# Kernel optimization log

Measured on AMD Instinct MI355X. Metric: run time of the kernel, lower is better.

The kernel has to match this reference:

```python
import jax, jax.numpy as jnp
import numpy as np

B, S, E, H = 8, 1024, 768, 12
D = E // H  # per-head dim


def setup_inputs() -> dict:
    key = jax.random.key(0)
    ks = jax.random.split(key, 9)
    glorot = lambda k: jax.random.normal(k, (E, E), jnp.float32) * np.sqrt(2.0 / (E + E))
    return {
        "inputs": jax.random.normal(ks[0], (B, S, E), jnp.float32),
        "Wq": glorot(ks[1]), "bq": jnp.zeros((E,), jnp.float32),
        "Wk": glorot(ks[2]), "bk": jnp.zeros((E,), jnp.float32),
        "Wv": glorot(ks[3]), "bv": jnp.zeros((E,), jnp.float32),
        "Wo": glorot(ks[4]), "bo": jnp.zeros((E,), jnp.float32),
    }


def reference(inputs, Wq, bq, Wk, bk, Wv, bv, Wo, bo):
    b, s, e = inputs.shape
    # QKV projections then split heads: [B,S,E] -> [B,H,S,D]
    def heads(x):
        return x.reshape(b, s, H, D).transpose(0, 2, 1, 3)
    q = heads(inputs @ Wq + bq)
    k = heads(inputs @ Wk + bk)
    v = heads(inputs @ Wv + bv)
    scale = 1.0 / jnp.sqrt(jnp.asarray(D, inputs.dtype))
    scores = jnp.einsum("bhqd,bhkd->bhqk", q, k) * scale
    weights = jax.nn.softmax(scores, axis=-1)  # attn_drop rate 0 -> identity
    attn = jnp.einsum("bhqk,bhkd->bhqd", weights, v)
    concat = attn.transpose(0, 2, 1, 3).reshape(b, s, e)
    out = concat @ Wo + bo  # proj_drop rate 0 -> identity
    return out
```

## Files before the change

### kernel.cpp

```cpp
#include <hip/hip_runtime.h>
#include <math.h>

#define BB 8
#define SS 1024
#define EE 768
#define HH 12
#define DD 64
#define MM (BB*SS)

typedef __attribute__((ext_vector_type(8))) short short8;
typedef __attribute__((ext_vector_type(4))) short short4v;
typedef __attribute__((ext_vector_type(4))) float f32x4;
typedef __attribute__((ext_vector_type(4))) int int4v;

static __device__ __forceinline__ short f2bf(float x) {
    unsigned u = __float_as_uint(x);
    u += 0x7fffu + ((u >> 16) & 1u);
    return (short)(u >> 16);
}
static __device__ __forceinline__ short f2bf_fast(float x) {
    return (short)((__float_as_uint(x) + 0x8000u) >> 16);
}

static __device__ __forceinline__ int cvtpk_bf16(float lo, float hi) {
    int r;
    asm("v_cvt_pk_bf16_f32 %0, %1, %2" : "=v"(r) : "v"(lo), "v"(hi));
    return r;
}
static __device__ __forceinline__ short8 i4_to_s8(int4v v) {
    union { int4v i; short8 s; } u; u.i = v; return u.s;
}

static __device__ __forceinline__ void gload_lds16(const void* g, void* l) {
    __builtin_amdgcn_global_load_lds((__attribute__((address_space(1))) void*)g,
                                     (__attribute__((address_space(3))) void*)l,
                                     16, 0, 0);
}

#define BAR __builtin_amdgcn_s_barrier()
#define VMW(n) asm volatile("s_waitcnt vmcnt(" #n ")" ::: "memory")

__global__ __launch_bounds__(256)
void cast_x(const float* __restrict__ src, short* __restrict__ dst) {
    const long i = ((long)blockIdx.x * 256 + threadIdx.x) * 4;
    float4 v = *(const float4*)&src[i];
    short4v o;
    o.x = f2bf(v.x); o.y = f2bf(v.y); o.z = f2bf(v.z); o.w = f2bf(v.w);
    *(short4v*)&dst[i] = o;
}

__global__ __launch_bounds__(256)
void wcast_t(const float* __restrict__ W0, const float* __restrict__ W1,
             const float* __restrict__ W2, const float* __restrict__ W3,
             short* __restrict__ Wt) {
    __shared__ short T[64][72];
    const int z = blockIdx.z;
    const float* sp = (z == 0) ? W0 : (z == 1) ? W1 : (z == 2) ? W2 : W3;
    short* dp = Wt + (long)z * EE * EE;
    const int i0 = blockIdx.y * 64;
    const int j0 = blockIdx.x * 64;
    const int tid = threadIdx.x;
#pragma unroll
    for (int rep = 0; rep < 4; ++rep) {
        const int r = (tid >> 4) + rep * 16;
        const int c = (tid & 15) * 4;
        float4 v = *(const float4*)&sp[(long)(i0 + r) * EE + j0 + c];
        T[c + 0][r] = f2bf(v.x);
        T[c + 1][r] = f2bf(v.y);
        T[c + 2][r] = f2bf(v.z);
        T[c + 3][r] = f2bf(v.w);
    }
    __syncthreads();
#pragma unroll
    for (int rep = 0; rep < 4; ++rep) {
        const int rr = (tid >> 4) + rep * 16;
        const int cc = (tid & 15) * 4;
        short4v o;
        o.x = T[rr][cc + 0]; o.y = T[rr][cc + 1];
        o.z = T[rr][cc + 2]; o.w = T[rr][cc + 3];
        *(short4v*)&dp[(long)(j0 + rr) * EE + i0 + cc] = o;
    }
}

#define GEMM_CORE(Abase, Bbase, row0, col0)                                     \
    f32x4 acc[4][4];                                                            \
    _Pragma("unroll") for (int i = 0; i < 4; ++i)                               \
        _Pragma("unroll") for (int j = 0; j < 4; ++j)                           \
            acc[i][j] = (f32x4){0.f, 0.f, 0.f, 0.f};                            \
    const int rm = (w & 1) * 64, cn = (w >> 1) * 64;                            \
    for (int k0 = 0; k0 < EE; k0 += 64) {                                       \
        __syncthreads();                                                        \
        _Pragma("unroll") for (int i = 0; i < 4; ++i) {                         \
            const int chunk = w * 256 + i * 64 + lane;                          \
            const int r = chunk >> 3;                                          \
            const int cs = (((chunk & 7) ^ (r & 7)) << 3);                      \
            short* ldsA = Al + (w * 256 + i * 64) * 8;                          \
            short* ldsB = Bl + (w * 256 + i * 64) * 8;                          \
            gload_lds16(&Abase[(long)(row0 + r) * EE + k0 + cs], ldsA);         \
            gload_lds16(&Bbase[(long)(col0 + r) * EE + k0 + cs], ldsB);         \
        }                                                                       \
        __syncthreads();                                                        \
        _Pragma("unroll") for (int ks = 0; ks < 2; ++ks) {                      \
            short8 af[4], bf[4];                                                \
            _Pragma("unroll") for (int t = 0; t < 4; ++t)                       \
                af[t] = *(const short8*)&Al[(rm + t * 16 + m) * 64 +            \
                                            (((ks * 4 + quad) ^ (m & 7)) << 3)]; \
            _Pragma("unroll") for (int t = 0; t < 4; ++t)                       \
                bf[t] = *(const short8*)&Bl[(cn + t * 16 + m) * 64 +            \
                                            (((ks * 4 + quad) ^ (m & 7)) << 3)]; \
            _Pragma("unroll") for (int mt = 0; mt < 4; ++mt)                    \
                _Pragma("unroll") for (int nt = 0; nt < 4; ++nt)                \
                    acc[mt][nt] = __builtin_amdgcn_mfma_f32_16x16x32_bf16(      \
                        af[mt], bf[nt], acc[mt][nt], 0, 0, 0);                  \
        }                                                                       \
    }

#define QSCALE 0.1803368801111204f

#define STG1(Ld, Gbase, gr0, k0)                                              \
    do {                                                                      \
        const int r_ = tid >> 3;                                              \
        const int cs_ = ((tid & 7) ^ (r_ & 7)) << 3;                          \
        gload_lds16(&(Gbase)[(long)((gr0) + r_) * EE + (k0) + cs_],           \
                    (Ld) + w * 512);                                          \
    } while (0)

#define QKV_RDA(Ld, mb)                                                       \
    _Pragma("unroll") for (int t = 0; t < 4; ++t)                             \
        _Pragma("unroll") for (int ks = 0; ks < 2; ++ks)                      \
            af[t][ks] = *(const short8*)&(Ld)[(wr * 128 + ((mb) + t) * 16 + m) * 64 + \
                                              (((ks * 4 + quad) ^ (m & 7)) << 3)];

#define QKV_RDB(Ld)                                                           \
    _Pragma("unroll") for (int t = 0; t < 2; ++t)                             \
        _Pragma("unroll") for (int ks = 0; ks < 2; ++ks)                      \
            bf[t][ks] = *(const short8*)&(Ld)[(wc * 32 + t * 16 + m) * 64 +   \
                                              (((ks * 4 + quad) ^ (m & 7)) << 3)];

#define QKV_MF(mb)                                                            \
    __builtin_amdgcn_s_setprio(1);                                            \
    _Pragma("unroll") for (int mq = 0; mq < 4; ++mq)                          \
        _Pragma("unroll") for (int nq = 0; nq < 2; ++nq)                      \
            _Pragma("unroll") for (int ks = 0; ks < 2; ++ks)                  \
                acc[(mb) + mq][nq] = __builtin_amdgcn_mfma_f32_16x16x32_bf16( \
                    af[mq][ks], bf[nq][ks], acc[(mb) + mq][nq], 0, 0, 0);     \
    __builtin_amdgcn_s_setprio(0);

__global__ __launch_bounds__(512, 2)
void gemm_qkv(const short* __restrict__ Xb, const short* __restrict__ Wt,
              const float* __restrict__ bq, const float* __restrict__ bk,
              const float* __restrict__ bv,
              short* __restrict__ Qb, short* __restrict__ Kb,
              short* __restrict__ Vb) {
    __shared__ short SMEM[49152];
    short* const Ae = SMEM;
    short* const Ao = SMEM + 16384;
    short* const Be = SMEM + 32768;
    short* const Bo = SMEM + 40960;

    const int tid = threadIdx.x;
    const int w = tid >> 6;
    const int m = tid & 15, quad = (tid & 63) >> 4;
    const int wr = w >> 2, wc = w & 3;

    const int flat = blockIdx.x + 18 * blockIdx.y;
    const int id   = (flat & 7) * 72 + (flat >> 3);
    const int lcl  = id % 72;
    const int rt   = (id / 72) * 4 + (lcl & 3);
    const int ct   = lcl >> 2;
    const int row0 = rt * 256;
    const int wsel = ct / 6;
    const int col0w = (ct % 6) * 128;
    const short* Wsel = Wt + (long)wsel * EE * EE;
    const float* bias = (wsel == 0) ? bq : (wsel == 1) ? bk : bv;

    f32x4 acc[8][2];
#pragma unroll
    for (int i = 0; i < 8; ++i)
#pragma unroll
        for (int j = 0; j < 2; ++j) acc[i][j] = (f32x4){0.f, 0.f, 0.f, 0.f};

    STG1(Ae + 0,     Xb,   row0 + 0,    0);
    STG1(Ae + 8192,  Xb,   row0 + 128,  0);
    STG1(Be + 0,     Wsel, col0w + 0,   0);
    STG1(Be + 4096,  Wsel, col0w + 64,  0);
    STG1(Ae + 4096,  Xb,   row0 + 64,   0);
    STG1(Ae + 12288, Xb,   row0 + 192,  0);
    STG1(Bo + 0,     Wsel, col0w + 0,   64);
    STG1(Bo + 4096,  Wsel, col0w + 64,  64);
    STG1(Ao + 0,     Xb,   row0 + 0,    64);
    STG1(Ao + 8192,  Xb,   row0 + 128,  64);
    VMW(6);
    BAR;

#pragma unroll 1
    for (int it = 0; it < 6; ++it) {
        const int kO1 = (2 * it + 1) * 64;
        const int t2 = 2 * it + 2, t3 = 2 * it + 3;
        const int kE2 = (t2 < 12 ? t2 : 11) * 64;
        const int kO3 = (t3 < 12 ? t3 : 11) * 64;
        short8 af[4][2], bf[2][2];
        QKV_RDA(Ae, 0);
        QKV_RDB(Be);
        STG1(Ao + 4096,  Xb, row0 + 64,  kO1);
        STG1(Ao + 12288, Xb, row0 + 192, kO1);
        BAR;
        QKV_MF(0);
        VMW(6);
        BAR;
        QKV_RDA(Ae, 4);
        STG1(Be + 0,     Wsel, col0w + 0,  kE2);
        STG1(Be + 4096,  Wsel, col0w + 64, kE2);
        STG1(Ae + 0,     Xb,   row0 + 0,   kE2);
        STG1(Ae + 8192,  Xb,   row0 + 128, kE2);
        BAR;
        QKV_MF(4);
        VMW(6);
        BAR;
        QKV_RDA(Ao, 0);
        QKV_RDB(Bo);
        STG1(Ae + 4096,  Xb, row0 + 64,  kE2);
        STG1(Ae + 12288, Xb, row0 + 192, kE2);
        BAR;
        QKV_MF(0);
        VMW(6);
        BAR;
        QKV_RDA(Ao, 4);
        STG1(Bo + 0,     Wsel, col0w + 0,  kO3);
        STG1(Bo + 4096,  Wsel, col0w + 64, kO3);
        STG1(Ao + 0,     Xb,   row0 + 0,   kO3);
        STG1(Ao + 8192,  Xb,   row0 + 128, kO3);
        BAR;
        QKV_MF(4);
        VMW(6);
        BAR;
    }

    VMW(0);
    __syncthreads();
    const int b = row0 >> 10, s0 = row0 & 1023;
    short* EP = SMEM;

    if (wsel < 2) {
        const float scale = (wsel == 0) ? QSCALE : 1.0f;
        short* QK = (wsel == 0) ? Qb : Kb;
#pragma unroll
        for (int nt = 0; nt < 2; ++nt) {
            const float bvv = bias[col0w + wc * 32 + nt * 16 + m];
#pragma unroll
            for (int mt = 0; mt < 8; ++mt)
#pragma unroll
                for (int r = 0; r < 4; ++r)
                    EP[(wr * 128 + mt * 16 + quad * 4 + r) * 136 + wc * 32 + nt * 16 + m] =
                        f2bf((acc[mt][nt][r] + bvv) * scale);
        }
        __syncthreads();
#pragma unroll
        for (int rep = 0; rep < 8; ++rep) {
            const int chunk = tid + rep * 512;
            const int row = chunk >> 4;
            const int cc = (chunk & 15) * 8;
            const int colg = col0w + cc;
            const int h = colg >> 6, d = colg & 63;
            short8 v = *(const short8*)&EP[row * 136 + cc];
            *(short8*)&QK[((long)(b * HH + h) * SS + s0 + row) * DD + d] = v;
        }
    } else {
#pragma unroll
        for (int nt = 0; nt < 2; ++nt) {
            const float bvv = bias[col0w + wc * 32 + nt * 16 + m];
#pragma unroll
            for (int mt = 0; mt < 8; ++mt) {
                short4v o;
                o.x = f2bf(acc[mt][nt][0] + bvv);
                o.y = f2bf(acc[mt][nt][1] + bvv);
                o.z = f2bf(acc[mt][nt][2] + bvv);
                o.w = f2bf(acc[mt][nt][3] + bvv);
                *(short4v*)&EP[(wc * 32 + nt * 16 + m) * 264 + wr * 128 + mt * 16 + quad * 4] = o;
            }
        }
        __syncthreads();
#pragma unroll
        for (int rep = 0; rep < 8; ++rep) {
            const int chunk = tid + rep * 512;
            const int col = chunk >> 5;
            const int sc8 = (chunk & 31) * 8;
            const int colg = col0w + col;
            const int h = colg >> 6, d = colg & 63;
            short8 v = *(const short8*)&EP[col * 264 + sc8];
            *(short8*)&Vb[((long)(b * HH + h) * DD + d) * SS + s0 + sc8] = v;
        }
    }
}

__global__ __launch_bounds__(256)
void gemm_proj(const short* __restrict__ Cb, const short* __restrict__ WoT,
               const float* __restrict__ bo, float* __restrict__ out) {
    __shared__ short Al[128 * 64];
    __shared__ short Bl[128 * 64];
    const int tid = threadIdx.x, w = tid >> 6, lane = tid & 63;
    const int m = lane & 15, quad = lane >> 4;

    const int flat = blockIdx.x + 6 * blockIdx.y;
    const int id   = (flat & 7) * 48 + (flat >> 3);
    const int xcd  = id / 48;
    const int lcl  = id % 48;
    const int row0 = (xcd * 8 + (lcl & 7)) * 128;
    const int col0 = (lcl >> 3) * 128;

    GEMM_CORE(Cb, WoT, row0, col0)

#pragma unroll
    for (int nt = 0; nt < 4; ++nt) {
        const int colg = col0 + cn + nt * 16 + m;
        const float bvv = bo[colg];
#pragma unroll
        for (int mt = 0; mt < 4; ++mt)
#pragma unroll
            for (int r = 0; r < 4; ++r) {
                const int srow = row0 + rm + mt * 16 + quad * 4 + r;
                out[(long)srow * EE + colg] = acc[mt][nt][r] + bvv;
            }
    }
}

#define ATTN_STAGE(Kdst, Vdst, k0)                                            \
    do {                                                                      \
        _Pragma("unroll") for (int i = 0; i < 2; ++i) {                       \
            const int chunk = w * 128 + i * 64 + l;                           \
            const int r = chunk >> 3;                                         \
            const int cs = ((chunk & 7) ^ (r & 7)) << 3;                      \
            gload_lds16(&Kg[(long)((k0) + r) * DD + cs],                      \
                        (Kdst) + (w * 128 + i * 64) * 8);                     \
            gload_lds16(&Vg[(long)r * SS + (k0) + cs],                        \
                        (Vdst) + (w * 128 + i * 64) * 8);                     \
        }                                                                     \
    } while (0)

#define ATTN_COMPUTE(Kbuf, Vbuf)                                              \
    do {                                                                      \
        f32x4 sc[2][4];                                                       \
        __builtin_amdgcn_s_setprio(1);                                        \
        _Pragma("unroll") for (int nt = 0; nt < 4; ++nt) {                    \
            const short* kb = (Kbuf) + (nt * 16 + m) * 64;                    \
            short8 a0 = *(const short8*)&kb[(quad ^ (m & 7)) << 3];           \
            short8 a1 = *(const short8*)&kb[((4 + quad) ^ (m & 7)) << 3];     \
            _Pragma("unroll") for (int g = 0; g < 2; ++g) {                   \
                f32x4 a = (f32x4){0.f, 0.f, 0.f, 0.f};                        \
                a = __builtin_amdgcn_mfma_f32_16x16x32_bf16(a0, aq[g][0], a, 0, 0, 0); \
                a = __builtin_amdgcn_mfma_f32_16x16x32_bf16(a1, aq[g][1], a, 0, 0, 0); \
                sc[g][nt] = a;                                                \
            }                                                                 \
        }                                                                     \
        __builtin_amdgcn_s_setprio(0);                                        \
        _Pragma("unroll") for (int g = 0; g < 2; ++g)                         \
            _Pragma("unroll") for (int nt = 0; nt < 4; ++nt)                  \
                _Pragma("unroll") for (int r = 0; r < 4; ++r)                 \
                    sc[g][nt][r] = __builtin_amdgcn_exp2f(sc[g][nt][r]);      \
        short8 ap[2][2];                                                      \
        _Pragma("unroll") for (int g = 0; g < 2; ++g)                         \
            _Pragma("unroll") for (int hf = 0; hf < 2; ++hf) {                \
                int4v wv;                                                     \
                wv.x = cvtpk_bf16(sc[g][2 * hf + 0][0], sc[g][2 * hf + 0][1]); \
                wv.y = cvtpk_bf16(sc[g][2 * hf + 0][2], sc[g][2 * hf + 0][3]); \
                wv.z = cvtpk_bf16(sc[g][2 * hf + 1][0], sc[g][2 * hf + 1][1]); \
                wv.w = cvtpk_bf16(sc[g][2 * hf + 1][2], sc[g][2 * hf + 1][3]); \
                ap[g][hf] = i4_to_s8(wv);                                     \
            }                                                                 \
        __builtin_amdgcn_s_setprio(1);                                        \
        _Pragma("unroll") for (int g = 0; g < 2; ++g) {                       \
            lacc[g] = __builtin_amdgcn_mfma_f32_16x16x32_bf16(ap[g][0], ones, lacc[g], 0, 0, 0); \
            lacc[g] = __builtin_amdgcn_mfma_f32_16x16x32_bf16(ap[g][1], ones, lacc[g], 0, 0, 0); \
        }                                                                     \
        const int rsw = m & 7, hb = (quad & 1) * 4;                           \
        _Pragma("unroll") for (int dt = 0; dt < 4; ++dt) {                    \
            const short* vb = (Vbuf) + (dt * 16 + m) * 64;                    \
            short4v l0 = *(const short4v*)&vb[((((quad >> 1) + 0) ^ rsw) << 3) + hb]; \
            short4v h0 = *(const short4v*)&vb[((((quad >> 1) + 2) ^ rsw) << 3) + hb]; \
            short4v l1 = *(const short4v*)&vb[((((quad >> 1) + 4) ^ rsw) << 3) + hb]; \
            short4v h1 = *(const short4v*)&vb[((((quad >> 1) + 6) ^ rsw) << 3) + hb]; \
            short8 b0 = __builtin_shufflevector(l0, h0, 0, 1, 2, 3, 4, 5, 6, 7); \
            short8 b1 = __builtin_shufflevector(l1, h1, 0, 1, 2, 3, 4, 5, 6, 7); \
            _Pragma("unroll") for (int g = 0; g < 2; ++g) {                   \
                O[g][dt] = __builtin_amdgcn_mfma_f32_16x16x32_bf16(ap[g][0], b0, O[g][dt], 0, 0, 0); \
                O[g][dt] = __builtin_amdgcn_mfma_f32_16x16x32_bf16(ap[g][1], b1, O[g][dt], 0, 0, 0); \
            }                                                                 \
        }                                                                     \
        __builtin_amdgcn_s_setprio(0);                                        \
    } while (0)

__global__ __launch_bounds__(256)
void attn_mfma(const short* __restrict__ Q,
               const short* __restrict__ K,
               const short* __restrict__ Vt,
               short* __restrict__ out) {
    __shared__ short K0l[64 * 64];
    __shared__ short K1l[64 * 64];
    __shared__ short V0l[64 * 64];
    __shared__ short V1l[64 * 64];

    const int tid  = threadIdx.x;
    const int w    = tid >> 6;
    const int l    = tid & 63;
    const int m    = l & 15;
    const int quad = l >> 4;

    const int flat = blockIdx.x + 8 * blockIdx.y + 96 * blockIdx.z;
    const int id   = (flat & 7) * 96 + (flat >> 3);
    const int qt   = id & 7;
    const int bh   = id >> 3;
    const int b    = bh / HH;
    const int h    = bh % HH;
    const int q0   = qt * 128;

    const short* Qg = Q  + (long)bh * SS * DD;
    const short* Kg = K  + (long)bh * SS * DD;
    const short* Vg = Vt + (long)bh * DD * SS;

    short8 aq[2][2];
#pragma unroll
    for (int g = 0; g < 2; ++g) {
        const int row = q0 + w * 32 + g * 16 + m;
        aq[g][0] = *(const short8*)(Qg + (long)row * DD + quad * 8);
        aq[g][1] = *(const short8*)(Qg + (long)row * DD + 32 + quad * 8);
    }

    short8 ones;
#pragma unroll
    for (int i = 0; i < 8; ++i) ones[i] = (short)0x3F80;

    f32x4 O[2][4], lacc[2];
#pragma unroll
    for (int g = 0; g < 2; ++g) {
        lacc[g] = (f32x4){0.f, 0.f, 0.f, 0.f};
#pragma unroll
        for (int dt = 0; dt < 4; ++dt) O[g][dt] = (f32x4){0.f, 0.f, 0.f, 0.f};
    }

    ATTN_STAGE(K0l, V0l, 0);
    __syncthreads();

#pragma unroll 1
    for (int kt2 = 0; kt2 < 8; ++kt2) {
        const int k0 = kt2 * 128;
        ATTN_STAGE(K1l, V1l, k0 + 64);
        ATTN_COMPUTE(K0l, V0l);
        __syncthreads();
        if (kt2 < 7) ATTN_STAGE(K0l, V0l, k0 + 128);
        ATTN_COMPUTE(K1l, V1l);
        __syncthreads();
    }

#pragma unroll
    for (int g = 0; g < 2; ++g)
#pragma unroll
        for (int r = 0; r < 4; ++r) {
            const float inv = 1.0f / lacc[g][r];
            const int qo = q0 + w * 32 + g * 16 + quad * 4 + r;
            short* orow = out + ((long)(b * SS + qo)) * EE + h * DD;
#pragma unroll
            for (int dt = 0; dt < 4; ++dt)
                orow[dt * 16 + m] = f2bf(O[g][dt][r] * inv);
        }
}

extern "C" void kernel_launch(void* const* d_in, const int* in_sizes, int n_in,
                              void* d_out, int out_size, void* d_ws, size_t ws_size,
                              hipStream_t stream) {
    const float* X  = (const float*)d_in[0];
    const float* Wq = (const float*)d_in[1];
    const float* bq = (const float*)d_in[2];
    const float* Wk = (const float*)d_in[3];
    const float* bk = (const float*)d_in[4];
    const float* Wv = (const float*)d_in[5];
    const float* bv = (const float*)d_in[6];
    const float* Wo = (const float*)d_in[7];
    const float* bo = (const float*)d_in[8];

    const long SEG = (long)BB * HH * SS * DD;
    const long WSEG = (long)EE * EE;
    short* Xb = (short*)d_ws;
    short* Wt = Xb + SEG;
    short* Qb = Wt + 4 * WSEG;
    short* Kb = Qb + SEG;
    short* Vb = Kb + SEG;
    short* Cb = Vb + SEG;

    cast_x<<<dim3(MM * EE / 4 / 256), 256, 0, stream>>>(X, Xb);
    wcast_t<<<dim3(12, 12, 4), 256, 0, stream>>>(Wq, Wk, Wv, Wo, Wt);

    gemm_qkv<<<dim3(18, 32), 512, 0, stream>>>(Xb, Wt, bq, bk, bv, Qb, Kb, Vb);

    attn_mfma<<<dim3(SS / 128, HH, BB), 256, 0, stream>>>(Qb, Kb, Vb, Cb);

    gemm_proj<<<dim3(6, 64), 256, 0, stream>>>(Cb, Wt + 3 * WSEG, bo,
                                               (float*)d_out);
}
```

Measured before the change: 197.7 us.

## Merge cast kernels into one launch and single-buffer QKV weight tiles

Folds the input cast and the weight cast/transpose into one prep kernel, removing a launch. In the QKV GEMM, the B (weight) tile drops from double to single buffering, shrinking LDS from 96KB to 80KB. Occupancy hint rises from 2 to 4 blocks, and the waitcnt schedule changes to vmcnt(2) with some waits removed. With one B buffer, the weight load for the next K step must finish before its reads, which reduces prefetch depth and adds a risk of races or stalls.

```diff
diff --git a/kernel.cpp b/kernel.cpp
--- a/kernel.cpp
+++ b/kernel.cpp
@@ -41,25 +41,27 @@
 #define VMW(n) asm volatile("s_waitcnt vmcnt(" #n ")" ::: "memory")
 
 __global__ __launch_bounds__(256)
-void cast_x(const float* __restrict__ src, short* __restrict__ dst) {
-    const long i = ((long)blockIdx.x * 256 + threadIdx.x) * 4;
-    float4 v = *(const float4*)&src[i];
-    short4v o;
-    o.x = f2bf(v.x); o.y = f2bf(v.y); o.z = f2bf(v.z); o.w = f2bf(v.w);
-    *(short4v*)&dst[i] = o;
-}
-
-__global__ __launch_bounds__(256)
-void wcast_t(const float* __restrict__ W0, const float* __restrict__ W1,
-             const float* __restrict__ W2, const float* __restrict__ W3,
-             short* __restrict__ Wt) {
+void prep(const float* __restrict__ X, short* __restrict__ Xb,
+          const float* __restrict__ W0, const float* __restrict__ W1,
+          const float* __restrict__ W2, const float* __restrict__ W3,
+          short* __restrict__ Wt) {
+    const int tid = threadIdx.x;
+    if (blockIdx.x < 6144) {
+        const long i = ((long)blockIdx.x * 256 + tid) * 4;
+        float4 v = *(const float4*)&X[i];
+        short4v o;
+        o.x = f2bf(v.x); o.y = f2bf(v.y); o.z = f2bf(v.z); o.w = f2bf(v.w);
+        *(short4v*)&Xb[i] = o;
+        return;
+    }
     __shared__ short T[64][72];
-    const int z = blockIdx.z;
+    const int id = blockIdx.x - 6144;
+    const int z  = id / 144;
+    const int r2 = id % 144;
+    const int i0 = (r2 / 12) * 64;
+    const int j0 = (r2 % 12) * 64;
     const float* sp = (z == 0) ? W0 : (z == 1) ? W1 : (z == 2) ? W2 : W3;
     short* dp = Wt + (long)z * EE * EE;
-    const int i0 = blockIdx.y * 64;
-    const int j0 = blockIdx.x * 64;
-    const int tid = threadIdx.x;
 #pragma unroll
     for (int rep = 0; rep < 4; ++rep) {
         const int r = (tid >> 4) + rep * 16;
@@ -146,17 +148,16 @@
                     af[mq][ks], bf[nq][ks], acc[(mb) + mq][nq], 0, 0, 0);     \
     __builtin_amdgcn_s_setprio(0);
 
-__global__ __launch_bounds__(512, 2)
+__global__ __launch_bounds__(512, 4)
 void gemm_qkv(const short* __restrict__ Xb, const short* __restrict__ Wt,
               const float* __restrict__ bq, const float* __restrict__ bk,
               const float* __restrict__ bv,
               short* __restrict__ Qb, short* __restrict__ Kb,
               short* __restrict__ Vb) {
-    __shared__ short SMEM[49152];
+    __shared__ short SMEM[40960];
     short* const Ae = SMEM;
     short* const Ao = SMEM + 16384;
-    short* const Be = SMEM + 32768;
-    short* const Bo = SMEM + 40960;
+    short* const Bl = SMEM + 32768;
 
     const int tid = threadIdx.x;
     const int w = tid >> 6;
@@ -182,15 +183,13 @@
 
     STG1(Ae + 0,     Xb,   row0 + 0,    0);
     STG1(Ae + 8192,  Xb,   row0 + 128,  0);
-    STG1(Be + 0,     Wsel, col0w + 0,   0);
-    STG1(Be + 4096,  Wsel, col0w + 64,  0);
     STG1(Ae + 4096,  Xb,   row0 + 64,   0);
     STG1(Ae + 12288, Xb,   row0 + 192,  0);
-    STG1(Bo + 0,     Wsel, col0w + 0,   64);
-    STG1(Bo + 4096,  Wsel, col0w + 64,  64);
+    STG1(Bl + 0,     Wsel, col0w + 0,   0);
+    STG1(Bl + 4096,  Wsel, col0w + 64,  0);
     STG1(Ao + 0,     Xb,   row0 + 0,    64);
     STG1(Ao + 8192,  Xb,   row0 + 128,  64);
-    VMW(6);
+    VMW(2);
     BAR;
 
 #pragma unroll 1
@@ -201,38 +200,36 @@
         const int kO3 = (t3 < 12 ? t3 : 11) * 64;
         short8 af[4][2], bf[2][2];
         QKV_RDA(Ae, 0);
-        QKV_RDB(Be);
+        QKV_RDB(Bl);
         STG1(Ao + 4096,  Xb, row0 + 64,  kO1);
         STG1(Ao + 12288, Xb, row0 + 192, kO1);
         BAR;
         QKV_MF(0);
-        VMW(6);
         BAR;
         QKV_RDA(Ae, 4);
-        STG1(Be + 0,     Wsel, col0w + 0,  kE2);
-        STG1(Be + 4096,  Wsel, col0w + 64, kE2);
+        STG1(Bl + 0,     Wsel, col0w + 0,  kO1);
+        STG1(Bl + 4096,  Wsel, col0w + 64, kO1);
         STG1(Ae + 0,     Xb,   row0 + 0,   kE2);
         STG1(Ae + 8192,  Xb,   row0 + 128, kE2);
         BAR;
         QKV_MF(4);
-        VMW(6);
+        VMW(2);
         BAR;
         QKV_RDA(Ao, 0);
-        QKV_RDB(Bo);
+        QKV_RDB(Bl);
         STG1(Ae + 4096,  Xb, row0 + 64,  kE2);
         STG1(Ae + 12288, Xb, row0 + 192, kE2);
         BAR;
         QKV_MF(0);
-        VMW(6);
         BAR;
         QKV_RDA(Ao, 4);
-        STG1(Bo + 0,     Wsel, col0w + 0,  kO3);
-        STG1(Bo + 4096,  Wsel, col0w + 64, kO3);
+        STG1(Bl + 0,     Wsel, col0w + 0,  kE2);
+        STG1(Bl + 4096,  Wsel, col0w + 64, kE2);
         STG1(Ao + 0,     Xb,   row0 + 0,   kO3);
         STG1(Ao + 8192,  Xb,   row0 + 128, kO3);
         BAR;
         QKV_MF(4);
-        VMW(6);
+        VMW(2);
         BAR;
     }
 
@@ -486,8 +483,7 @@
     short* Vb = Kb + SEG;
     short* Cb = Vb + SEG;
 
-    cast_x<<<dim3(MM * EE / 4 / 256), 256, 0, stream>>>(X, Xb);
-    wcast_t<<<dim3(12, 12, 4), 256, 0, stream>>>(Wq, Wk, Wv, Wo, Wt);
+    prep<<<dim3(6720), 256, 0, stream>>>(X, Xb, Wq, Wk, Wv, Wo, Wt);
 
     gemm_qkv<<<dim3(18, 32), 512, 0, stream>>>(Xb, Wt, bq, bk, bv, Qb, Kb, Vb);
 
```

New measurement: 213.8 us. 8.1% more time.
